# Performance work log

Measured on AMD Instinct MI355X. Metric: run time of the kernel, lower is better.

The kernel has to match this reference:

```python
import jax, jax.numpy as jnp
import numpy as np

N_NODES = 16384
N_EDGES = 65536
B = 256
L = 1000
BN_EPS = 1e-5


def _bn_last(h, g, b, m, v):
    # BatchNorm1d in eval mode over last (feature) axis
    return (h - m) / jnp.sqrt(v + BN_EPS) * g + b


def _bn_chan(h, g, b, m, v):
    # BatchNorm1d in eval mode over channel axis of [N, C, W]
    inv = g / jnp.sqrt(v + BN_EPS)
    return (h - m[None, :, None]) * inv[None, :, None] + b[None, :, None]


def _conv1d(x, W, b):
    # x: [N, C, W], W: [O, I, K], stride 1, VALID
    y = jax.lax.conv_general_dilated(x, W, (1,), 'VALID',
                                     dimension_numbers=('NCH', 'OIH', 'NCH'))
    return y + b[None, :, None]


def _forward(x, g1_W1, g1_b1, g1_W2, g1_b2, gW1, gb1, gW2, gb2,
             bn_gamma, bn_beta, bn_mean, bn_var, fcxd_W, fcxd_b, embed,
             c1_W, c1_b, c2_W, c2_b, c3_W, c3_b,
             cbn_gamma, cbn_beta, cbn_mean, cbn_var, fcxc_W, fcxc_b,
             bnfc_gamma, bnfc_beta, bnfc_mean, bnfc_var,
             fc1_W, fc1_b, fc2_W, fc2_b, out_W, out_b,
             edge_index, batch, target):
    src, dst = edge_index[0], edge_index[1]
    # GIN layer 1: out_i = MLP(x_i + sum_{j->i} x_j)  (eps = 0)
    agg = jax.ops.segment_sum(x[src], dst, num_segments=N_NODES)
    h = x + agg
    h = jnp.maximum(h @ g1_W1 + g1_b1, 0.0) @ g1_W2 + g1_b2
    h = _bn_last(jnp.maximum(h, 0.0), bn_gamma[0], bn_beta[0], bn_mean[0], bn_var[0])
    # GIN layers 2..5 (stacked params)
    for i in range(4):
        agg = jax.ops.segment_sum(h[src], dst, num_segments=N_NODES)
        t = h + agg
        t = jnp.maximum(t @ gW1[i] + gb1[i], 0.0) @ gW2[i] + gb2[i]
        h = _bn_last(jnp.maximum(t, 0.0), bn_gamma[i + 1], bn_beta[i + 1],
                     bn_mean[i + 1], bn_var[i + 1])
    # global_add_pool over graph ids
    pooled = jax.ops.segment_sum(h, batch, num_segments=B)          # [B, 32]
    xd = jnp.maximum(pooled @ fcxd_W + fcxd_b, 0.0)                 # [B, 128] (dropout: eval)
    # protein branch
    emb = embed[target]                                             # [B, L, 128]
    xd2 = jnp.broadcast_to(xd[:, None, :], (B, L, xd.shape[-1]))
    xc = jnp.concatenate([emb, xd2], axis=-1).transpose(0, 2, 1)    # [B, 256, L]
    conv_params = [(c1_W, c1_b), (c2_W, c2_b), (c3_W, c3_b)]
    for i in range(3):
        xc = _conv1d(xc, conv_params[i][0], conv_params[i][1])
        xc = jnp.maximum(_bn_chan(xc, cbn_gamma[i], cbn_beta[i],
                                  cbn_mean[i], cbn_var[i]), 0.0)
    xcm = jnp.max(xc, axis=-1)                                      # global max pool -> [B, 32]
    xcf = jnp.maximum(_bn_last(xcm @ fcxc_W + fcxc_b,
                               bnfc_gamma, bnfc_beta, bnfc_mean, bnfc_var), 0.0)
    z = jnp.concatenate([xd, xcf], axis=1)                          # [B, 256]
    z = jnp.maximum(z @ fc1_W + fc1_b, 0.0)
    z = jnp.maximum(z @ fc2_W + fc2_b, 0.0)
    return z @ out_W + out_b                                        # [B, 1]


def setup_inputs() -> dict:
    key = jax.random.key(0)
    ks = list(jax.random.split(key, 48))
    it = iter(range(48))
    f32 = jnp.float32

    def rn(sh, s=0.1):
        return jax.random.normal(ks[next(it)], sh, dtype=f32) * s

    def un(sh):
        return jax.random.uniform(ks[next(it)], sh, dtype=f32, minval=0.5, maxval=1.5)

    inp = {}
    inp['x'] = jax.random.normal(ks[next(it)], (N_NODES, 78), dtype=f32)
    inp['edge_index'] = jax.random.randint(ks[next(it)], (2, N_EDGES), 0, N_NODES, dtype=jnp.int32)
    inp['batch'] = jnp.sort(jax.random.randint(ks[next(it)], (N_NODES,), 0, B, dtype=jnp.int32))
    inp['target'] = jax.random.randint(ks[next(it)], (B, L), 0, 26, dtype=jnp.int32)
    inp['g1_W1'] = rn((78, 32)); inp['g1_b1'] = rn((32,))
    inp['g1_W2'] = rn((32, 32)); inp['g1_b2'] = rn((32,))
    inp['gW1'] = rn((4, 32, 32)); inp['gb1'] = rn((4, 32))
    inp['gW2'] = rn((4, 32, 32)); inp['gb2'] = rn((4, 32))
    inp['bn_gamma'] = un((5, 32)); inp['bn_beta'] = rn((5, 32))
    inp['bn_mean'] = rn((5, 32)); inp['bn_var'] = un((5, 32))
    inp['fcxd_W'] = rn((32, 128)); inp['fcxd_b'] = rn((128,))
    inp['embed'] = rn((26, 128), 1.0)
    inp['c1_W'] = rn((32, 256, 16)); inp['c1_b'] = rn((32,))
    inp['c2_W'] = rn((32, 32, 16)); inp['c2_b'] = rn((32,))
    inp['c3_W'] = rn((32, 32, 16)); inp['c3_b'] = rn((32,))
    inp['cbn_gamma'] = un((3, 32)); inp['cbn_beta'] = rn((3, 32))
    inp['cbn_mean'] = rn((3, 32)); inp['cbn_var'] = un((3, 32))
    inp['fcxc_W'] = rn((32, 128)); inp['fcxc_b'] = rn((128,))
    inp['bnfc_gamma'] = un((128,)); inp['bnfc_beta'] = rn((128,))
    inp['bnfc_mean'] = rn((128,)); inp['bnfc_var'] = un((128,))
    inp['fc1_W'] = rn((256, 1024)); inp['fc1_b'] = rn((1024,))
    inp['fc2_W'] = rn((1024, 256)); inp['fc2_b'] = rn((256,))
    inp['out_W'] = rn((256, 1)); inp['out_b'] = rn((1,))
    return inp


def reference(x, edge_index, batch, target, g1_W1, g1_b1, g1_W2, g1_b2,
              gW1, gb1, gW2, gb2, bn_gamma, bn_beta, bn_mean, bn_var,
              fcxd_W, fcxd_b, embed, c1_W, c1_b, c2_W, c2_b, c3_W, c3_b,
              cbn_gamma, cbn_beta, cbn_mean, cbn_var, fcxc_W, fcxc_b,
              bnfc_gamma, bnfc_beta, bnfc_mean, bnfc_var,
              fc1_W, fc1_b, fc2_W, fc2_b, out_W, out_b):
    return _forward(x, g1_W1, g1_b1, g1_W2, g1_b2, gW1, gb1, gW2, gb2,
                    bn_gamma, bn_beta, bn_mean, bn_var, fcxd_W, fcxd_b, embed,
                    c1_W, c1_b, c2_W, c2_b, c3_W, c3_b,
                    cbn_gamma, cbn_beta, cbn_mean, cbn_var, fcxc_W, fcxc_b,
                    bnfc_gamma, bnfc_beta, bnfc_mean, bnfc_var,
                    fc1_W, fc1_b, fc2_W, fc2_b, out_W, out_b,
                    edge_index, batch, target)
```

## Files before the change

kernel.cpp:

```cpp
#include <hip/hip_runtime.h>
#include <hip/hip_bf16.h>

typedef __hip_bfloat16 bf16;
__device__ __forceinline__ float b2f(bf16 v){ return __bfloat162float(v); }

typedef __attribute__((ext_vector_type(8))) short s8v;
typedef __attribute__((ext_vector_type(4))) float f4v;

#define N_NODES 16384
#define N_EDGES 65536
#define NB 256
#define LSEQ 1000
#define BN_EPS 1e-5f
#define W1O 985
#define W2O 970
#define W3O 955
#define C1S 988
#define C2S 976

__device__ int g_isf32;

__device__ __forceinline__ float LD(const void* p, int i, int f){
    return f ? ((const float*)p)[i] : b2f(((const bf16*)p)[i]);
}

__device__ __forceinline__ unsigned short f2b(float x){
    unsigned u = __float_as_uint(x);
    return (unsigned short)((u + 0x7FFFu + ((u >> 16) & 1u)) >> 16);
}
__device__ __forceinline__ float bb2f(unsigned short h){
    return __uint_as_float(((unsigned)h) << 16);
}

__global__ void k_dtype(const void* x){
    if (threadIdx.x != 0 || blockIdx.x != 0) return;
    const unsigned short* u = (const unsigned short*)x;
    int insane = 0;
    for (int i = 0; i < 512; i++){
        unsigned short h = u[i];
        int ex = (h >> 7) & 0xFF;
        if (!(h == 0 || (ex >= 96 && ex <= 142))) insane++;
    }
    g_isf32 = (insane > 50) ? 1 : 0;
}

__device__ float g_hA[N_NODES*32];
__device__ float g_hB[N_NODES*32];
__device__ float g_xd[NB*128];
__device__ float g_P[16*26*32];
__device__ float g_wsum[32*128];
__device__ float g_xdb[NB*32];
__device__ float g_xcm[NB*32];
__device__ float g_c1o[NB*32*C1S];
__device__ float g_c2o[NB*32*C2S];
__device__ __attribute__((aligned(16))) unsigned short g_wf[2][32768];
__device__ int g_deg[N_NODES];
__device__ int g_cur[N_NODES];
__device__ int g_rowptr[N_NODES + 1];
__device__ int g_csrc[N_EDGES];
__device__ int g_gstart[NB + 1];

__global__ void k_zero(){
    int i = blockIdx.x*256 + threadIdx.x;
    if (i < N_NODES) g_deg[i] = 0;
    else g_xcm[i - N_NODES] = 0.f;
}

__global__ void k_count(const int* __restrict__ ei){
    int e = blockIdx.x*256 + threadIdx.x;
    atomicAdd(&g_deg[ei[N_EDGES + e]], 1);
}
__global__ __launch_bounds__(1024) void k_scan(){
    __shared__ int part[1024];
    int t = threadIdx.x;
    int base = t*16;
    int s = 0;
    #pragma unroll
    for (int i = 0; i < 16; i++) s += g_deg[base + i];
    part[t] = s;
    __syncthreads();
    for (int off = 1; off < 1024; off <<= 1){
        int v = (t >= off) ? part[t - off] : 0;
        __syncthreads();
        part[t] += v;
        __syncthreads();
    }
    int run = (t == 0) ? 0 : part[t - 1];
    for (int i = 0; i < 16; i++){
        g_rowptr[base + i] = run;
        g_cur[base + i] = run;
        run += g_deg[base + i];
    }
    if (t == 1023) g_rowptr[N_NODES] = run;
}
__global__ void k_fill(const int* __restrict__ ei){
    int e = blockIdx.x*256 + threadIdx.x;
    int d = ei[N_EDGES + e];
    int slot = atomicAdd(&g_cur[d], 1);
    g_csrc[slot] = ei[e];
}
__global__ void k_ranges(const int* __restrict__ batch){
    int b = threadIdx.x;
    int lo = 0, hi = N_NODES;
    while (lo < hi){ int mid = (lo + hi) >> 1; if (batch[mid] < b) lo = mid + 1; else hi = mid; }
    g_gstart[b] = lo;
    if (b == 0) g_gstart[NB] = N_NODES;
}

__global__ void k_wpack(const void* w2, const void* w3){
    const int F = g_isf32;
    int idx = blockIdx.x*256 + threadIdx.x;
    int sel = idx >> 15;
    int r = idx & 32767;
    int j = r & 7;
    int lane = (r >> 3) & 63;
    int hl = (r >> 9) & 1;
    int ogrp = (r >> 10) & 1;
    int ktg = r >> 11;
    int c = (lane >> 4)*8 + j;
    int o = ogrp*16 + (lane & 15);
    const void* Wt = sel ? w3 : w2;
    float wv = LD(Wt, o*512 + c*16 + ktg, F);
    unsigned short h = f2b(wv);
    g_wf[sel][r] = hl ? f2b(wv - bb2f(h)) : h;
}


__global__ __launch_bounds__(256) void k_proj78(const void* x, const void* W1)
{
    const int F = g_isf32;
    __shared__ float sW1[78*32];
    __shared__ float sx[8][78];
    int tid = threadIdx.x;
    for (int i = tid; i < 78*32; i += 256) sW1[i] = LD(W1, i, F);
    int nodeBase = blockIdx.x * 8;
    for (int i = tid; i < 8*78; i += 256){
        int ln = i / 78, f = i - ln*78;
        sx[ln][f] = LD(x, (nodeBase + ln)*78 + f, F);
    }
    __syncthreads();
    int ln = tid >> 5, j = tid & 31;
    float a = 0.f;
    #pragma unroll 6
    for (int i = 0; i < 78; i++) a += sx[ln][i] * sW1[i*32 + j];
    g_hA[(nodeBase + ln)*32 + j] = a;
}

__device__ __forceinline__ float csr_gather(const float* hin, int n, int j){
    int rs = g_rowptr[n];
    int deg = g_rowptr[n + 1] - rs;
    float agg = 0.f;
    for (int base = 0; base < deg; base += 32){
        int cnt = deg - base; if (cnt > 32) cnt = 32;
        int myidx = (j < cnt) ? g_csrc[rs + base + j] : 0;
        for (int e = 0; e < cnt; e++){
            int src = __shfl(myidx, e, 32);
            agg += hin[src*32 + j];
        }
    }
    return agg;
}

__global__ __launch_bounds__(256) void k_gin1b(
    const void* b1, const void* W2, const void* b2,
    const void* bng, const void* bnb, const void* bnm, const void* bnv)
{
    const int F = g_isf32;
    __shared__ float sW2[32*32];
    __shared__ float sb1[32], sb2[32], sA[32], sB[32];
    __shared__ float st[8][32];
    int tid = threadIdx.x;
    for (int i = tid; i < 1024; i += 256) sW2[i] = LD(W2, i, F);
    if (tid < 32){
        sb1[tid] = LD(b1, tid, F); sb2[tid] = LD(b2, tid, F);
        float inv = LD(bng, tid, F) * rsqrtf(LD(bnv, tid, F) + BN_EPS);
        sA[tid] = inv;
        sB[tid] = LD(bnb, tid, F) - LD(bnm, tid, F) * inv;
    }
    __syncthreads();
    int ln = tid >> 5, j = tid & 31;
    int n = blockIdx.x*8 + ln;
    float agg = csr_gather(g_hA, n, j);
    st[ln][j] = fmaxf(g_hA[n*32 + j] + agg + sb1[j], 0.f);
    __syncthreads();
    float t2 = sb2[j];
    #pragma unroll
    for (int i = 0; i < 32; i++) t2 += st[ln][i] * sW2[i*32 + j];
    t2 = fmaxf(t2, 0.f);
    g_hB[n*32 + j] = t2 * sA[j] + sB[j];
}

__global__ __launch_bounds__(256) void k_gin32L(
    const void* W1, const void* b1, const void* W2, const void* b2,
    const void* bng, const void* bnb, const void* bnm, const void* bnv, int l)
{
    const int F = g_isf32;
    const float* hin = (l & 1) ? g_hA : g_hB;
    float* hout = (l & 1) ? g_hB : g_hA;
    const int oW = l*1024, ob = l*32, obn = (l+1)*32;
    __shared__ float sW1[32*32], sW2[32*32];
    __shared__ float sb1[32], sb2[32], sA[32], sB[32];
    __shared__ float sh[8][32], st[8][32];
    int tid = threadIdx.x;
    for (int i = tid; i < 1024; i += 256){ sW1[i] = LD(W1, oW + i, F); sW2[i] = LD(W2, oW + i, F); }
    if (tid < 32){
        sb1[tid] = LD(b1, ob + tid, F); sb2[tid] = LD(b2, ob + tid, F);
        float inv = LD(bng, obn + tid, F) * rsqrtf(LD(bnv, obn + tid, F) + BN_EPS);
        sA[tid] = inv;
        sB[tid] = LD(bnb, obn + tid, F) - LD(bnm, obn + tid, F) * inv;
    }
    int ln = tid >> 5, j = tid & 31;
    int n = blockIdx.x*8 + ln;
    float agg = csr_gather(hin, n, j);
    sh[ln][j] = hin[n*32 + j] + agg;
    __syncthreads();
    float t1 = sb1[j];
    #pragma unroll
    for (int i = 0; i < 32; i++) t1 += sh[ln][i] * sW1[i*32 + j];
    st[ln][j] = fmaxf(t1, 0.f);
    __syncthreads();
    float t2 = sb2[j];
    #pragma unroll
    for (int i = 0; i < 32; i++) t2 += st[ln][i] * sW2[i*32 + j];
    t2 = fmaxf(t2, 0.f);
    hout[n*32 + j] = t2 * sA[j] + sB[j];
}

__global__ __launch_bounds__(256) void k_poolxd(const void* W, const void* bias,
                                                const void* c1b){
    const int F = g_isf32;
    __shared__ float red[8][32];
    __shared__ float sxd[128];
    int b = blockIdx.x, tid = threadIdx.x;
    int j = tid & 31, sub = tid >> 5;
    int s = g_gstart[b], e = g_gstart[b + 1];
    float a = 0.f;
    for (int n = s + sub; n < e; n += 8) a += g_hB[n*32 + j];
    red[sub][j] = a;
    __syncthreads();
    if (sub == 0){
        red[0][j] = red[0][j] + red[1][j] + red[2][j] + red[3][j]
                  + red[4][j] + red[5][j] + red[6][j] + red[7][j];
    }
    __syncthreads();
    if (tid < 128){
        float acc = LD(bias, tid, F);
        #pragma unroll
        for (int i = 0; i < 32; i++) acc += red[0][i] * LD(W, i*128 + tid, F);
        float xdv = fmaxf(acc, 0.f);
        g_xd[b*128 + tid] = xdv;
        sxd[tid] = xdv;
    }
    __syncthreads();
    if (tid < 32){
        float a2 = LD(c1b, tid, F);
        for (int c = 0; c < 128; c++) a2 += sxd[c] * g_wsum[tid*128 + c];
        g_xdb[b*32 + tid] = a2;
    }
}


__global__ void k_Pw(const void* embed, const void* c1W){
    const int F = g_isf32;
    if (blockIdx.x < 52){
        int idx = blockIdx.x*256 + threadIdx.x;
        if (idx >= 16*26*32) return;
        int o = idx & 31;
        int t = (idx >> 5) % 26;
        int k = idx / (32*26);
        float a = 0.f;
        for (int c = 0; c < 128; c++)
            a += LD(embed, t*128 + c, F) * LD(c1W, o*4096 + c*16 + k, F);
        g_P[(k*26 + t)*32 + o] = a;
    } else {
        int idx = (blockIdx.x - 52)*256 + threadIdx.x;
        int o = idx >> 7, c = idx & 127;
        float a = 0.f;
        #pragma unroll
        for (int k = 0; k < 16; k++) a += LD(c1W, o*4096 + (128 + c)*16 + k, F);
        g_wsum[o*128 + c] = a;
    }
}

__global__ __launch_bounds__(256) void k_conv1L(
    const int* __restrict__ target,
    const void* g, const void* be, const void* m, const void* v, int obn)
{
    const int F = g_isf32;
    __shared__ int   stg[LSEQ];
    __shared__ float sxb[32], sA[32], sB[32];
    int b = blockIdx.x >> 2, q = blockIdx.x & 3;
    int tid = threadIdx.x;
    for (int i = tid; i < LSEQ; i += 256) stg[i] = target[b*LSEQ + i];
    if (tid < 32){
        sxb[tid] = g_xdb[b*32 + tid];
        float inv = LD(g, obn + tid, F) * rsqrtf(LD(v, obn + tid, F) + BN_EPS);
        sA[tid] = inv;
        sB[tid] = LD(be, obn + tid, F) - LD(m, obn + tid, F) * inv;
    }
    __syncthreads();
    int o = tid & 31, wsub = tid >> 5;
    float xb = sxb[o], aa = sA[o], bb = sB[o];
    int wlo = q*248;
    int whi = (q == 3) ? W1O : wlo + 248;
    for (int w = wlo + wsub; w < whi; w += 8){
        float a = xb;
        #pragma unroll
        for (int k = 0; k < 16; k++)
            a += g_P[(k*26 + stg[w + k])*32 + o];
        g_c1o[(b*32 + o)*C1S + w] = fmaxf(a * aa + bb, 0.f);
    }
}


#define CT_W 128
#define CT_R 144
#define CPAD 40

__global__ __launch_bounds__(256) void k_cmfma(
    int sel, int Wvalid, int Wout, int inStride,
    const void* bias, const void* g, const void* be,
    const void* m, const void* v, int obn)
{
    const int F = g_isf32;
    const float* in = (sel == 0) ? g_c1o : g_c2o;
    __shared__ __attribute__((aligned(16))) unsigned short sAh[CT_R*CPAD];
    __shared__ __attribute__((aligned(16))) unsigned short sAl[CT_R*CPAD];
    __shared__ float sSc[32], sOf[32];
    int tid = threadIdx.x;
    int b = blockIdx.x >> 3;
    int tile = blockIdx.x & 7;
    int wbase = tile * CT_W;

    for (int c = 0; c < 32; c++){
        const float* src = in + (b*32 + c)*inStride;
        if (tid < CT_R){
            int wg_ = wbase + tid;
            float xv = (wg_ < Wvalid) ? src[wg_] : 0.f;
            unsigned short h = f2b(xv);
            sAh[tid*CPAD + c] = h;
            sAl[tid*CPAD + c] = f2b(xv - bb2f(h));
        }
    }
    if (tid < 32){
        float inv = LD(g, obn + tid, F) * rsqrtf(LD(v, obn + tid, F) + BN_EPS);
        sSc[tid] = inv;
        sOf[tid] = LD(be, obn + tid, F) + (LD(bias, tid, F) - LD(m, obn + tid, F)) * inv;
    }
    __syncthreads();

    int lane = tid & 63;
    int wv = tid >> 6;
    int ml = lane & 15, quad = lane >> 4;
    int wgrp = wv & 1;
    int ogrp = wv >> 1;

    const s8v* wfb = (const s8v*)&g_wf[sel][0] + ogrp*128 + lane;

    f4v acc[4];
    #pragma unroll
    for (int mt = 0; mt < 4; mt++) acc[mt] = (f4v){0.f, 0.f, 0.f, 0.f};

    s8v nbh = wfb[0], nbl = wfb[64];
    for (int ktg = 0; ktg < 16; ktg++){
        s8v bh = nbh, bl = nbl;
        if (ktg < 15){
            nbh = wfb[(ktg + 1)*256];
            nbl = wfb[(ktg + 1)*256 + 64];
        }
        #pragma unroll
        for (int mt = 0; mt < 4; mt++){
            int row = wgrp*64 + mt*16 + ml + ktg;
            const int aidx = row*CPAD + quad*8;
            s8v ah = *(const s8v*)&sAh[aidx];
            s8v al = *(const s8v*)&sAl[aidx];
            acc[mt] = __builtin_amdgcn_mfma_f32_16x16x32_bf16(ah, bh, acc[mt], 0, 0, 0);
            acc[mt] = __builtin_amdgcn_mfma_f32_16x16x32_bf16(ah, bl, acc[mt], 0, 0, 0);
            acc[mt] = __builtin_amdgcn_mfma_f32_16x16x32_bf16(al, bh, acc[mt], 0, 0, 0);
        }
    }

    int o = ogrp*16 + ml;
    float sc = sSc[o], of = sOf[o];
    #pragma unroll
    for (int mt = 0; mt < 4; mt++){
        int w0 = wbase + wgrp*64 + mt*16 + quad*4;
        f4v a = acc[mt];
        float y0 = fmaxf(a.x*sc + of, 0.f);
        float y1 = fmaxf(a.y*sc + of, 0.f);
        float y2 = fmaxf(a.z*sc + of, 0.f);
        float y3 = fmaxf(a.w*sc + of, 0.f);
        if (sel == 0){
            float* dst = &g_c2o[(b*32 + o)*C2S + w0];
            if (w0 + 3 < Wout){
                *(float4*)dst = make_float4(y0, y1, y2, y3);
            } else if (w0 < Wout){
                dst[0] = y0;
                if (w0+1 < Wout) dst[1] = y1;
                if (w0+2 < Wout) dst[2] = y2;
                if (w0+3 < Wout) dst[3] = y3;
            }
        } else {
            if (w0 < Wout){
                float mx = y0;
                if (w0+1 < Wout) mx = fmaxf(mx, y1);
                if (w0+2 < Wout) mx = fmaxf(mx, y2);
                if (w0+3 < Wout) mx = fmaxf(mx, y3);
                atomicMax((int*)&g_xcm[b*32 + o], __float_as_int(mx));
            }
        }
    }
}


__global__ __launch_bounds__(1024) void k_tail(
    const void* fcxcW, const void* fcxcb,
    const void* bg, const void* bb, const void* bm, const void* bv,
    const void* fc1W, const void* fc1b,
    const void* fc2W, const void* fc2b,
    const void* outW, const void* outb, void* out)
{
    const int F = g_isf32;
    __shared__ float sz[256];
    __shared__ float z1s[1024];
    __shared__ float sp[4][256];
    int b = blockIdx.x, t = threadIdx.x;
    if (t < 128) sz[t] = g_xd[b*128 + t];
    else if (t < 256){
        int j = t - 128;
        float a = LD(fcxcb, j, F);
        #pragma unroll
        for (int i = 0; i < 32; i++) a += g_xcm[b*32 + i] * LD(fcxcW, i*128 + j, F);
        float inv = LD(bg, j, F) * rsqrtf(LD(bv, j, F) + BN_EPS);
        a = (a - LD(bm, j, F)) * inv + LD(bb, j, F);
        sz[t] = fmaxf(a, 0.f);
    }
    __syncthreads();
    float a = LD(fc1b, t, F);
    for (int i = 0; i < 256; i++) a += sz[i] * LD(fc1W, i*1024 + t, F);
    z1s[t] = fmaxf(a, 0.f);
    __syncthreads();
    int j = t & 255, kq = t >> 8;
    float a2 = 0.f;
    #pragma unroll 8
    for (int i = 0; i < 256; i++)
        a2 += z1s[kq*256 + i] * LD(fc2W, (kq*256 + i)*256 + j, F);
    sp[kq][j] = a2;
    __syncthreads();
    if (t < 256){
        float z2 = fmaxf(sp[0][t] + sp[1][t] + sp[2][t] + sp[3][t] + LD(fc2b, t, F), 0.f);
        sp[0][t] = z2 * LD(outW, t, F);
    }
    __syncthreads();
    for (int s = 128; s > 0; s >>= 1){
        if (t < s) sp[0][t] += sp[0][t + s];
        __syncthreads();
    }
    if (t == 0){
        float r = sp[0][0] + LD(outb, 0, F);
        if (F) ((float*)out)[b] = r;
        else   ((bf16*)out)[b] = __float2bfloat16(r);
    }
}


extern "C" void kernel_launch(void* const* d_in, const int* in_sizes, int n_in,
                              void* d_out, int out_size, void* d_ws, size_t ws_size,
                              hipStream_t stream)
{
    (void)in_sizes; (void)n_in; (void)out_size; (void)d_ws; (void)ws_size;
    const void* x      = d_in[0];
    const int*  ei     = (const int*)d_in[1];
    const int*  batch  = (const int*)d_in[2];
    const int*  target = (const int*)d_in[3];
    const void* g1W1 = d_in[4];  const void* g1b1 = d_in[5];
    const void* g1W2 = d_in[6];  const void* g1b2 = d_in[7];
    const void* gW1  = d_in[8];  const void* gb1  = d_in[9];
    const void* gW2  = d_in[10]; const void* gb2  = d_in[11];
    const void* bng  = d_in[12]; const void* bnb  = d_in[13];
    const void* bnm  = d_in[14]; const void* bnv  = d_in[15];
    const void* fcxdW = d_in[16]; const void* fcxdb = d_in[17];
    const void* embed = d_in[18];
    const void* c1W = d_in[19]; const void* c1b = d_in[20];
    const void* c2W = d_in[21]; const void* c2b = d_in[22];
    const void* c3W = d_in[23]; const void* c3b = d_in[24];
    const void* cbng = d_in[25]; const void* cbnb = d_in[26];
    const void* cbnm = d_in[27]; const void* cbnv = d_in[28];
    const void* fcxcW = d_in[29]; const void* fcxcb = d_in[30];
    const void* bnfcg = d_in[31]; const void* bnfcb = d_in[32];
    const void* bnfcm = d_in[33]; const void* bnfcv = d_in[34];
    const void* fc1W = d_in[35]; const void* fc1b = d_in[36];
    const void* fc2W = d_in[37]; const void* fc2b = d_in[38];
    const void* outW = d_in[39]; const void* outb = d_in[40];

    k_dtype<<<1, 64, 0, stream>>>(x);
    k_wpack<<<256, 256, 0, stream>>>(c2W, c3W);
    k_Pw<<<68, 256, 0, stream>>>(embed, c1W);

    k_zero<<<(N_NODES + NB*32)/256, 256, 0, stream>>>();
    k_count<<<N_EDGES/256, 256, 0, stream>>>(ei);
    k_scan<<<1, 1024, 0, stream>>>();
    k_fill<<<N_EDGES/256, 256, 0, stream>>>(ei);
    k_ranges<<<1, 256, 0, stream>>>(batch);

    k_proj78<<<N_NODES/8, 256, 0, stream>>>(x, g1W1);
    k_gin1b<<<N_NODES/8, 256, 0, stream>>>(g1b1, g1W2, g1b2, bng, bnb, bnm, bnv);
    for (int l = 0; l < 4; l++){
        k_gin32L<<<N_NODES/8, 256, 0, stream>>>(gW1, gb1, gW2, gb2,
                                                bng, bnb, bnm, bnv, l);
    }
    k_poolxd<<<NB, 256, 0, stream>>>(fcxdW, fcxdb, c1b);
    k_conv1L<<<NB*4, 256, 0, stream>>>(target, cbng, cbnb, cbnm, cbnv, 0);
    k_cmfma<<<NB*8, 256, 0, stream>>>(0, W1O, W2O, C1S,
                                      c2b, cbng, cbnb, cbnm, cbnv, 32);
    k_cmfma<<<NB*8, 256, 0, stream>>>(1, W2O, W3O, C2S,
                                      c3b, cbng, cbnb, cbnm, cbnv, 64);
    k_tail<<<NB, 1024, 0, stream>>>(fcxcW, fcxcb, bnfcg, bnfcb, bnfcm, bnfcv,
                                    fc1W, fc1b, fc2W, fc2b, outW, outb, d_out);
}
```

Measured before the change: 477.5 us.

## Fuse three conv layers into one tiled kernel keeping intermediates in LDS

Replaces the separate conv1 gather kernel and two MFMA conv kernels with one kernel per (batch, 128-wide tile). Each tile recomputes a halo of conv1 rows (160) and conv2 rows (144) and keeps them in shared memory as split bf16 hi/lo pairs. This removes the global round trips of the large fp32 conv1 and conv2 intermediates and two kernel launches. In exchange it adds redundant halo computation, more LDS per block (which may lower occupancy) and extra syncthreads barriers.

```diff
diff --git a/kernel.cpp b/kernel.cpp
--- a/kernel.cpp
+++ b/kernel.cpp
@@ -15,8 +15,6 @@
 #define W1O 985
 #define W2O 970
 #define W3O 955
-#define C1S 988
-#define C2S 976
 
 __device__ int g_isf32;
 
@@ -51,8 +49,6 @@
 __device__ float g_wsum[32*128];
 __device__ float g_xdb[NB*32];
 __device__ float g_xcm[NB*32];
-__device__ float g_c1o[NB*32*C1S];
-__device__ float g_c2o[NB*32*C2S];
 __device__ __attribute__((aligned(16))) unsigned short g_wf[2][32768];
 __device__ int g_deg[N_NODES];
 __device__ int g_cur[N_NODES];
@@ -282,70 +278,63 @@
     }
 }
 
-__global__ __launch_bounds__(256) void k_conv1L(
+
+#define FT_W 128
+#define C1R 160
+#define C2R 144
+#define CPAD 40
+#define STGN 176
+
+__global__ __launch_bounds__(256) void k_cfuse(
     const int* __restrict__ target,
-    const void* g, const void* be, const void* m, const void* v, int obn)
+    const void* g, const void* be, const void* m, const void* v,
+    const void* c2b, const void* c3b)
 {
     const int F = g_isf32;
-    __shared__ int   stg[LSEQ];
-    __shared__ float sxb[32], sA[32], sB[32];
-    int b = blockIdx.x >> 2, q = blockIdx.x & 3;
+    __shared__ int stg[STGN];
+    __shared__ __attribute__((aligned(16))) unsigned short sC1h[C1R*CPAD];
+    __shared__ __attribute__((aligned(16))) unsigned short sC1l[C1R*CPAD];
+    __shared__ __attribute__((aligned(16))) unsigned short sC2h[C2R*CPAD];
+    __shared__ __attribute__((aligned(16))) unsigned short sC2l[C2R*CPAD];
+    __shared__ float sxb[32], sA1[32], sB1[32], sSc2[32], sOf2[32], sSc3[32], sOf3[32];
+    int b = blockIdx.x >> 3;
+    int tile = blockIdx.x & 7;
+    int wbase = tile * FT_W;
     int tid = threadIdx.x;
-    for (int i = tid; i < LSEQ; i += 256) stg[i] = target[b*LSEQ + i];
+
+    for (int i = tid; i < STGN; i += 256){
+        int gi = wbase + i;
+        stg[i] = (gi < LSEQ) ? target[b*LSEQ + gi] : 0;
+    }
     if (tid < 32){
         sxb[tid] = g_xdb[b*32 + tid];
-        float inv = LD(g, obn + tid, F) * rsqrtf(LD(v, obn + tid, F) + BN_EPS);
-        sA[tid] = inv;
-        sB[tid] = LD(be, obn + tid, F) - LD(m, obn + tid, F) * inv;
-    }
-    __syncthreads();
-    int o = tid & 31, wsub = tid >> 5;
-    float xb = sxb[o], aa = sA[o], bb = sB[o];
-    int wlo = q*248;
-    int whi = (q == 3) ? W1O : wlo + 248;
-    for (int w = wlo + wsub; w < whi; w += 8){
-        float a = xb;
-        #pragma unroll
-        for (int k = 0; k < 16; k++)
-            a += g_P[(k*26 + stg[w + k])*32 + o];
-        g_c1o[(b*32 + o)*C1S + w] = fmaxf(a * aa + bb, 0.f);
-    }
-}
-
-
-#define CT_W 128
-#define CT_R 144
-#define CPAD 40
-
-__global__ __launch_bounds__(256) void k_cmfma(
-    int sel, int Wvalid, int Wout, int inStride,
-    const void* bias, const void* g, const void* be,
-    const void* m, const void* v, int obn)
-{
-    const int F = g_isf32;
-    const float* in = (sel == 0) ? g_c1o : g_c2o;
-    __shared__ __attribute__((aligned(16))) unsigned short sAh[CT_R*CPAD];
-    __shared__ __attribute__((aligned(16))) unsigned short sAl[CT_R*CPAD];
-    __shared__ float sSc[32], sOf[32];
-    int tid = threadIdx.x;
-    int b = blockIdx.x >> 3;
-    int tile = blockIdx.x & 7;
-    int wbase = tile * CT_W;
-
-    for (int c = 0; c < 32; c++){
-        const float* src = in + (b*32 + c)*inStride;
-        if (tid < CT_R){
-            int wg_ = wbase + tid;
-            float xv = (wg_ < Wvalid) ? src[wg_] : 0.f;
-            unsigned short h = f2b(xv);
-            sAh[tid*CPAD + c] = h;
-            sAl[tid*CPAD + c] = f2b(xv - bb2f(h));
+        float i1 = LD(g, tid, F) * rsqrtf(LD(v, tid, F) + BN_EPS);
+        sA1[tid] = i1;
+        sB1[tid] = LD(be, tid, F) - LD(m, tid, F) * i1;
+        float i2 = LD(g, 32 + tid, F) * rsqrtf(LD(v, 32 + tid, F) + BN_EPS);
+        sSc2[tid] = i2;
+        sOf2[tid] = LD(be, 32 + tid, F) + (LD(c2b, tid, F) - LD(m, 32 + tid, F)) * i2;
+        float i3 = LD(g, 64 + tid, F) * rsqrtf(LD(v, 64 + tid, F) + BN_EPS);
+        sSc3[tid] = i3;
+        sOf3[tid] = LD(be, 64 + tid, F) + (LD(c3b, tid, F) - LD(m, 64 + tid, F)) * i3;
+    }
+    __syncthreads();
+
+    {
+        int o = tid & 31, rsub = tid >> 5;
+        for (int r = rsub; r < C1R; r += 8){
+            float val = 0.f;
+            if (wbase + r < W1O){
+                float a = sxb[o];
+                #pragma unroll
+                for (int k = 0; k < 16; k++)
+                    a += g_P[(k*26 + stg[r + k])*32 + o];
+                val = fmaxf(a * sA1[o] + sB1[o], 0.f);
+            }
+            unsigned short h = f2b(val);
+            sC1h[r*CPAD + o] = h;
+            sC1l[r*CPAD + o] = f2b(val - bb2f(h));
         }
-    }
-    if (tid < 32){
-        float inv = LD(g, obn + tid, F) * rsqrtf(LD(v, obn + tid, F) + BN_EPS);
-        sSc[tid] = inv;
-        sOf[tid] = LD(be, obn + tid, F) + (LD(bias, tid, F) - LD(m, obn + tid, F)) * inv;
     }
     __syncthreads();
 
@@ -354,59 +343,86 @@
     int ml = lane & 15, quad = lane >> 4;
     int wgrp = wv & 1;
     int ogrp = wv >> 1;
-
-    const s8v* wfb = (const s8v*)&g_wf[sel][0] + ogrp*128 + lane;
-
-    f4v acc[4];
-    #pragma unroll
-    for (int mt = 0; mt < 4; mt++) acc[mt] = (f4v){0.f, 0.f, 0.f, 0.f};
-
-    s8v nbh = wfb[0], nbl = wfb[64];
-    for (int ktg = 0; ktg < 16; ktg++){
-        s8v bh = nbh, bl = nbl;
-        if (ktg < 15){
-            nbh = wfb[(ktg + 1)*256];
-            nbl = wfb[(ktg + 1)*256 + 64];
+    int oo = ogrp*16 + ml;
+
+    {
+        const s8v* wfb = (const s8v*)&g_wf[0][0] + ogrp*128 + lane;
+        int nmt = 5 - wgrp;
+        f4v acc[5];
+        #pragma unroll
+        for (int i = 0; i < 5; i++) acc[i] = (f4v){0.f,0.f,0.f,0.f};
+        s8v nbh = wfb[0], nbl = wfb[64];
+        for (int ktg = 0; ktg < 16; ktg++){
+            s8v bh = nbh, bl = nbl;
+            if (ktg < 15){ nbh = wfb[(ktg+1)*256]; nbl = wfb[(ktg+1)*256 + 64]; }
+            #pragma unroll
+            for (int i = 0; i < 5; i++){
+                if (i < nmt){
+                    int row = (wgrp + 2*i)*16 + ml + ktg;
+                    int aidx = row*CPAD + quad*8;
+                    s8v ah = *(const s8v*)&sC1h[aidx];
+                    s8v al = *(const s8v*)&sC1l[aidx];
+                    acc[i] = __builtin_amdgcn_mfma_f32_16x16x32_bf16(ah, bh, acc[i], 0, 0, 0);
+                    acc[i] = __builtin_amdgcn_mfma_f32_16x16x32_bf16(ah, bl, acc[i], 0, 0, 0);
+                    acc[i] = __builtin_amdgcn_mfma_f32_16x16x32_bf16(al, bh, acc[i], 0, 0, 0);
+                }
+            }
         }
+        float sc = sSc2[oo], of = sOf2[oo];
+        #pragma unroll
+        for (int i = 0; i < 5; i++){
+            if (i < nmt){
+                int mt = wgrp + 2*i;
+                f4v a = acc[i];
+                float ys[4] = {a.x, a.y, a.z, a.w};
+                #pragma unroll
+                for (int rr = 0; rr < 4; rr++){
+                    int row = mt*16 + quad*4 + rr;
+                    float y = fmaxf(ys[rr]*sc + of, 0.f);
+                    unsigned short h = f2b(y);
+                    sC2h[row*CPAD + oo] = h;
+                    sC2l[row*CPAD + oo] = f2b(y - bb2f(h));
+                }
+            }
+        }
+    }
+    __syncthreads();
+
+    {
+        const s8v* wfb = (const s8v*)&g_wf[1][0] + ogrp*128 + lane;
+        f4v acc[4];
+        #pragma unroll
+        for (int mt = 0; mt < 4; mt++) acc[mt] = (f4v){0.f,0.f,0.f,0.f};
+        s8v nbh = wfb[0], nbl = wfb[64];
+        for (int ktg = 0; ktg < 16; ktg++){
+            s8v bh = nbh, bl = nbl;
+            if (ktg < 15){ nbh = wfb[(ktg+1)*256]; nbl = wfb[(ktg+1)*256 + 64]; }
+            #pragma unroll
+            for (int mt = 0; mt < 4; mt++){
+                int row = wgrp*64 + mt*16 + ml + ktg;
+                int aidx = row*CPAD + quad*8;
+                s8v ah = *(const s8v*)&sC2h[aidx];
+                s8v al = *(const s8v*)&sC2l[aidx];
+                acc[mt] = __builtin_amdgcn_mfma_f32_16x16x32_bf16(ah, bh, acc[mt], 0, 0, 0);
+                acc[mt] = __builtin_amdgcn_mfma_f32_16x16x32_bf16(ah, bl, acc[mt], 0, 0, 0);
+                acc[mt] = __builtin_amdgcn_mfma_f32_16x16x32_bf16(al, bh, acc[mt], 0, 0, 0);
+            }
+        }
+        float sc = sSc3[oo], of = sOf3[oo];
         #pragma unroll
         for (int mt = 0; mt < 4; mt++){
-            int row = wgrp*64 + mt*16 + ml + ktg;
-            const int aidx = row*CPAD + quad*8;
-            s8v ah = *(const s8v*)&sAh[aidx];
-            s8v al = *(const s8v*)&sAl[aidx];
-            acc[mt] = __builtin_amdgcn_mfma_f32_16x16x32_bf16(ah, bh, acc[mt], 0, 0, 0);
-            acc[mt] = __builtin_amdgcn_mfma_f32_16x16x32_bf16(ah, bl, acc[mt], 0, 0, 0);
-            acc[mt] = __builtin_amdgcn_mfma_f32_16x16x32_bf16(al, bh, acc[mt], 0, 0, 0);
-        }
-    }
-
-    int o = ogrp*16 + ml;
-    float sc = sSc[o], of = sOf[o];
-    #pragma unroll
-    for (int mt = 0; mt < 4; mt++){
-        int w0 = wbase + wgrp*64 + mt*16 + quad*4;
-        f4v a = acc[mt];
-        float y0 = fmaxf(a.x*sc + of, 0.f);
-        float y1 = fmaxf(a.y*sc + of, 0.f);
-        float y2 = fmaxf(a.z*sc + of, 0.f);
-        float y3 = fmaxf(a.w*sc + of, 0.f);
-        if (sel == 0){
-            float* dst = &g_c2o[(b*32 + o)*C2S + w0];
-            if (w0 + 3 < Wout){
-                *(float4*)dst = make_float4(y0, y1, y2, y3);
-            } else if (w0 < Wout){
-                dst[0] = y0;
-                if (w0+1 < Wout) dst[1] = y1;
-                if (w0+2 < Wout) dst[2] = y2;
-                if (w0+3 < Wout) dst[3] = y3;
-            }
-        } else {
-            if (w0 < Wout){
+            int w0 = wbase + wgrp*64 + mt*16 + quad*4;
+            f4v a = acc[mt];
+            float y0 = fmaxf(a.x*sc + of, 0.f);
+            float y1 = fmaxf(a.y*sc + of, 0.f);
+            float y2 = fmaxf(a.z*sc + of, 0.f);
+            float y3 = fmaxf(a.w*sc + of, 0.f);
+            if (w0 < W3O){
                 float mx = y0;
-                if (w0+1 < Wout) mx = fmaxf(mx, y1);
-                if (w0+2 < Wout) mx = fmaxf(mx, y2);
-                if (w0+3 < Wout) mx = fmaxf(mx, y3);
-                atomicMax((int*)&g_xcm[b*32 + o], __float_as_int(mx));
+                if (w0+1 < W3O) mx = fmaxf(mx, y1);
+                if (w0+2 < W3O) mx = fmaxf(mx, y2);
+                if (w0+3 < W3O) mx = fmaxf(mx, y3);
+                atomicMax((int*)&g_xcm[b*32 + oo], __float_as_int(mx));
             }
         }
     }
@@ -510,11 +526,7 @@
                                                 bng, bnb, bnm, bnv, l);
     }
     k_poolxd<<<NB, 256, 0, stream>>>(fcxdW, fcxdb, c1b);
-    k_conv1L<<<NB*4, 256, 0, stream>>>(target, cbng, cbnb, cbnm, cbnv, 0);
-    k_cmfma<<<NB*8, 256, 0, stream>>>(0, W1O, W2O, C1S,
-                                      c2b, cbng, cbnb, cbnm, cbnv, 32);
-    k_cmfma<<<NB*8, 256, 0, stream>>>(1, W2O, W3O, C2S,
-                                      c3b, cbng, cbnb, cbnm, cbnv, 64);
+    k_cfuse<<<NB*8, 256, 0, stream>>>(target, cbng, cbnb, cbnm, cbnv, c2b, c3b);
     k_tail<<<NB, 1024, 0, stream>>>(fcxcW, fcxcb, bnfcg, bnfcb, bnfcm, bnfcv,
                                     fc1W, fc1b, fc2W, fc2b, outW, outb, d_out);
 }
```

Result: faster. 439.4 us (-8.0%).
